# Kernel optimization log

Measured on AMD Instinct MI355X. Metric: run time of the kernel, lower is better.

Reference implementation:

```python
import jax, jax.numpy as jnp
import numpy as np

B, D, V, T = 256, 1024, 32000, 64  # num_seqs, hidden dim, vocab, history len


def setup_inputs() -> dict:
    key = jax.random.key(0)
    ks = jax.random.split(key, 8)
    hidden = jax.random.normal(ks[0], (B, D), dtype=jnp.float32)
    embedding = jax.random.normal(ks[1], (V, D), dtype=jnp.float32) * (1.0 / np.sqrt(D))
    output_tokens = jax.random.randint(ks[2], (B, T), 0, V, dtype=jnp.int64)
    presence_penalties = jax.random.uniform(ks[3], (B,), dtype=jnp.float32)
    frequency_penalties = jax.random.uniform(ks[4], (B,), dtype=jnp.float32)
    temperatures = jax.random.uniform(ks[5], (B,), dtype=jnp.float32) + 0.5  # > eps
    top_ps = jax.random.uniform(ks[6], (B,), dtype=jnp.float32) * 0.5 + 0.5  # in [0.5, 1.0)
    top_ks = jax.random.randint(ks[7], (B,), 1, V, dtype=jnp.int64)
    return {
        "hidden": hidden,
        "embedding": embedding,
        "output_tokens": output_tokens,
        "presence_penalties": presence_penalties,
        "frequency_penalties": frequency_penalties,
        "temperatures": temperatures,
        "top_ps": top_ps,
        "top_ks": top_ks,
    }


def reference(hidden, embedding, output_tokens, presence_penalties,
              frequency_penalties, temperatures, top_ps, top_ks):
    # 1) logits = pruned hidden states @ embedding^T  -> [B, V]
    logits = jnp.einsum("bd,vd->bv", hidden, embedding)
    b, v = logits.shape

    # 2) presence/frequency penalties via per-row token histogram (np.bincount equiv)
    rows = jnp.broadcast_to(jnp.arange(b)[:, None], output_tokens.shape)
    counts = jnp.zeros((b, v), logits.dtype).at[rows, output_tokens].add(1.0)
    logits = logits - frequency_penalties[:, None] * counts \
                    - presence_penalties[:, None] * (counts > 0).astype(logits.dtype)

    # 3) temperature scaling
    logits = logits / temperatures[:, None]

    # 4) probabilities
    probs = jax.nn.softmax(logits, axis=-1)

    # 5) top-p / top-k: descending sort, cumsum masks, scatter back via inverse perm
    order = jnp.argsort(-probs, axis=-1)                       # descending order
    probs_sort = jnp.take_along_axis(probs, order, axis=-1)
    probs_cum = jnp.cumsum(probs_sort, axis=-1)
    top_p_mask = (probs_cum - probs_sort) > top_ps[:, None]
    top_k_mask = jnp.arange(v)[None, :] >= top_ks[:, None]
    probs_sort = jnp.where(top_p_mask | top_k_mask, 0.0, probs_sort)
    inv = jnp.argsort(order, axis=-1)
    filtered_probs = jnp.take_along_axis(probs_sort, inv, axis=-1)  # original order
    return filtered_probs
```

## Files before the change

kernel.cpp:

```cpp
#include <hip/hip_runtime.h>
#include <math.h>

#define NB 256
#define NV 32000
#define ND 1024
#define NT 64

#define GN 64
#define BSTR 40
#define NKB 64
#define AKBF 8192
#define NGBLK (NV / GN)
#define INV2048F 4.8828125e-4f

#define NBIN 1024
#define HSTR 1032
#define HTOT (4 * HSTR)
#define FIX2 4294967296.0
#define SMASK ((1ull << 48) - 1ull)
#define SMEM_BYTES (NV * 4 + HTOT * 4)

typedef _Float16 f16x8 __attribute__((ext_vector_type(8)));
typedef _Float16 f16x4 __attribute__((ext_vector_type(4)));
typedef float f32x16 __attribute__((ext_vector_type(16)));

struct RowP2 {
  unsigned long long basePack;
  unsigned long long toppZfix;
  unsigned pfx;
  int ktop;
  float invZ;
  unsigned ustar;
  int m;
  int cEq;
};

__device__ __forceinline__ unsigned mono_enc(float f) {
  unsigned u = __float_as_uint(f);
  return (u & 0x80000000u) ? ~u : (u | 0x80000000u);
}
__device__ __forceinline__ float mono_dec(unsigned u) {
  return (u & 0x80000000u) ? __uint_as_float(u & 0x7FFFFFFFu) : __uint_as_float(~u);
}

__global__ __launch_bounds__(256) void convert_A(const float* __restrict__ hidden,
                                                 _Float16* __restrict__ A3) {
  const int g = blockIdx.x * 256 + threadIdx.x;
  const int kb = g >> 10, rem = g & 1023, r = rem >> 2, c = rem & 3;
  const float4 a4 = *(const float4*)(hidden + (size_t)r * ND + kb * 16 + c * 4);
  const float v[4] = {a4.x, a4.y, a4.z, a4.w};
  f16x4 h4, q4;
#pragma unroll
  for (int q = 0; q < 4; q++) {
    const _Float16 hh = (_Float16)v[q];
    h4[q] = hh;
    q4[q] = (_Float16)((v[q] - (float)hh) * 2048.0f);
  }
  const int s = r >> 5, l31 = r & 31;
  const int lh = c >> 1, j4 = (c & 1) * 4;
  const int lane = l31 + (lh << 5);
  _Float16* base = A3 + (size_t)kb * AKBF;
  *(f16x4*)(base + ((s * 2 + 0) * 64 + lane) * 8 + j4) = h4;
  *(f16x4*)(base + ((s * 2 + 1) * 64 + lane) * 8 + j4) = q4;
}

__global__ __launch_bounds__(256, 2) void gemm_f16s(
    const float* __restrict__ Bm, const _Float16* __restrict__ A3,
    const float* __restrict__ temp, unsigned* __restrict__ rowmax,
    float* __restrict__ C) {
  __shared__ _Float16 Bls[2][GN * BSTR];
  __shared__ float s_invT[256];
  __shared__ unsigned s_pm[256];

  const int t = threadIdx.x;
  const int l = t & 63, w = t >> 6;
  const int n0 = blockIdx.x * GN;
  s_invT[t] = 1.0f / temp[t];
  s_pm[t] = 0u;

  f32x16 accH[2][2] = {};
  f32x16 accC[2][2] = {};

  const int bn = t >> 2, bk4 = (t & 3) * 4;
  const int l31 = l & 31, lh = l >> 5;
  const int ka = lh * 8;
  const int mb = w * 64;

  const float* browp = Bm + (size_t)(n0 + bn) * ND + bk4;
  const _Float16* aB = A3 + 2048 * w + l * 8;

  f16x8 eh0, eh1, eq0, eq1;
  f16x8 oh0, oh1, oq0, oq1;

#define LOADA(P, KB)                                                  \
  do {                                                                \
    const _Float16* ap_ = aB + (size_t)(KB) * AKBF;                   \
    P##h0 = *(const f16x8*)(ap_);                                     \
    P##q0 = *(const f16x8*)(ap_ + 512);                               \
    P##h1 = *(const f16x8*)(ap_ + 1024);                              \
    P##q1 = *(const f16x8*)(ap_ + 1536);                              \
  } while (0)

#define BCONV(BV, DST)                                                \
  do {                                                                \
    f16x4 h4_, q4_;                                                   \
    const float vv_[4] = {(BV).x, (BV).y, (BV).z, (BV).w};            \
    _Pragma("unroll") for (int j_ = 0; j_ < 4; j_++) {                \
      const _Float16 h_ = (_Float16)vv_[j_];                          \
      h4_[j_] = h_;                                                   \
      q4_[j_] = (_Float16)((vv_[j_] - (float)h_) * 2048.0f);          \
    }                                                                 \
    _Float16* prow_ = (DST) + bn * BSTR;                              \
    *(f16x4*)(prow_ + bk4) = h4_;                                     \
    *(f16x4*)(prow_ + 16 + bk4) = q4_;                                \
  } while (0)

#define COMPUTE(P, CUR)                                                                     \
  do {                                                                                      \
    const _Float16* Bp_ = &Bls[CUR][0] + (size_t)l31 * BSTR + ka;                           \
    f16x8 b0h_ = *(const f16x8*)(Bp_);                                                      \
    f16x8 b1h_ = *(const f16x8*)(Bp_ + 32 * BSTR);                                          \
    accH[0][0] = __builtin_amdgcn_mfma_f32_32x32x16_f16(P##h0, b0h_, accH[0][0], 0, 0, 0);  \
    accH[0][1] = __builtin_amdgcn_mfma_f32_32x32x16_f16(P##h0, b1h_, accH[0][1], 0, 0, 0);  \
    accH[1][0] = __builtin_amdgcn_mfma_f32_32x32x16_f16(P##h1, b0h_, accH[1][0], 0, 0, 0);  \
    accH[1][1] = __builtin_amdgcn_mfma_f32_32x32x16_f16(P##h1, b1h_, accH[1][1], 0, 0, 0);  \
    f16x8 b0q_ = *(const f16x8*)(Bp_ + 16);                                                 \
    f16x8 b1q_ = *(const f16x8*)(Bp_ + 32 * BSTR + 16);                                     \
    accC[0][0] = __builtin_amdgcn_mfma_f32_32x32x16_f16(P##h0, b0q_, accC[0][0], 0, 0, 0);  \
    accC[0][1] = __builtin_amdgcn_mfma_f32_32x32x16_f16(P##h0, b1q_, accC[0][1], 0, 0, 0);  \
    accC[1][0] = __builtin_amdgcn_mfma_f32_32x32x16_f16(P##h1, b0q_, accC[1][0], 0, 0, 0);  \
    accC[1][1] = __builtin_amdgcn_mfma_f32_32x32x16_f16(P##h1, b1q_, accC[1][1], 0, 0, 0);  \
    accC[0][0] = __builtin_amdgcn_mfma_f32_32x32x16_f16(P##q0, b0h_, accC[0][0], 0, 0, 0);  \
    accC[0][1] = __builtin_amdgcn_mfma_f32_32x32x16_f16(P##q0, b1h_, accC[0][1], 0, 0, 0);  \
    accC[1][0] = __builtin_amdgcn_mfma_f32_32x32x16_f16(P##q1, b0h_, accC[1][0], 0, 0, 0);  \
    accC[1][1] = __builtin_amdgcn_mfma_f32_32x32x16_f16(P##q1, b1h_, accC[1][1], 0, 0, 0);  \
  } while (0)

  LOADA(e, 0);
  __builtin_amdgcn_sched_barrier(0);
  float4 bv0 = *(const float4*)(browp);
  __builtin_amdgcn_sched_barrier(0);
  LOADA(o, 1);
  __builtin_amdgcn_sched_barrier(0);
  float4 bvA = *(const float4*)(browp + 16);
  __builtin_amdgcn_sched_barrier(0);
  BCONV(bv0, &Bls[0][0]);
  asm volatile("s_waitcnt lgkmcnt(0)\ns_barrier" ::: "memory");

  float4 bvB;
  for (int kb = 0; kb < 62; kb += 2) {
    COMPUTE(e, 0);
    __builtin_amdgcn_sched_barrier(0);
    LOADA(e, kb + 2);
    __builtin_amdgcn_sched_barrier(0);
    bvB = *(const float4*)(browp + (size_t)(kb + 2) * 16);
    __builtin_amdgcn_sched_barrier(0);
    BCONV(bvA, &Bls[1][0]);
    asm volatile("s_waitcnt lgkmcnt(0)\ns_barrier" ::: "memory");

    COMPUTE(o, 1);
    __builtin_amdgcn_sched_barrier(0);
    LOADA(o, kb + 3);
    __builtin_amdgcn_sched_barrier(0);
    bvA = *(const float4*)(browp + (size_t)(kb + 3) * 16);
    __builtin_amdgcn_sched_barrier(0);
    BCONV(bvB, &Bls[0][0]);
    asm volatile("s_waitcnt lgkmcnt(0)\ns_barrier" ::: "memory");
  }
  COMPUTE(e, 0);
  __builtin_amdgcn_sched_barrier(0);
  BCONV(bvA, &Bls[1][0]);
  asm volatile("s_waitcnt lgkmcnt(0)\ns_barrier" ::: "memory");
  COMPUTE(o, 1);

#undef LOADA
#undef BCONV
#undef COMPUTE

#pragma unroll
  for (int mi = 0; mi < 2; mi++) {
#pragma unroll
    for (int r = 0; r < 16; r++) {
      const int row = mb + mi * 32 + (r & 3) + 8 * (r >> 2) + 4 * lh;
      const float it = s_invT[row];
      float v0 = (accH[mi][0][r] + accC[mi][0][r] * INV2048F) * it;
      float v1 = (accH[mi][1][r] + accC[mi][1][r] * INV2048F) * it;
      C[(size_t)row * NV + n0 + l31] = v0;
      C[(size_t)row * NV + n0 + 32 + l31] = v1;
      float mx = fmaxf(v0, v1);
#pragma unroll
      for (int o = 1; o < 32; o <<= 1) mx = fmaxf(mx, __shfl_xor(mx, o));
      if (l31 == 0) atomicMax(&s_pm[row], mono_enc(mx));
    }
  }
  __syncthreads();
  atomicMax(&rowmax[t], s_pm[t]);
}

__global__ __launch_bounds__(1024) void sample_row(
    float* __restrict__ buf, const unsigned* __restrict__ rowmax,
    const int* __restrict__ toks, const float* __restrict__ pres,
    const float* __restrict__ freq, const float* __restrict__ temp,
    const float* __restrict__ topp_a, const int* __restrict__ topk_a) {
  extern __shared__ char smem[];
  float* e = (float*)smem;
  unsigned* hist = (unsigned*)(smem + NV * 4);
  unsigned long long* suf = (unsigned long long*)hist;
  __shared__ unsigned long long wtot16[16];
  __shared__ int s_tok[NT];
  __shared__ int s_bs;
  __shared__ RowP2 sp;

  const int b = blockIdx.x, t = threadIdx.x;
  const int cp = (t >> 6) & 1;
  unsigned* loP = hist + cp * HSTR;
  unsigned* hcP = hist + 2 * HSTR + cp * HSTR;
  float* row = buf + (size_t)b * NV;

#define HACC(K, BIN)                                                            \
  do {                                                                          \
    unsigned long long m_ = (unsigned long long)(((K) & 0x7FFFFFu) | 0x800000u);\
    const int sh_ = (int)((K) >> 23) - 118;                                     \
    const unsigned long long f_ =                                               \
        (sh_ >= 0) ? (m_ << sh_) : ((sh_ > -24) ? (m_ >> (-sh_)) : 0ull);       \
    const unsigned flo_ = (unsigned)f_;                                         \
    const unsigned old_ = atomicAdd(&loP[BIN], flo_);                           \
    const unsigned hc_ = 0x10000u + (unsigned)(f_ >> 32) +                      \
                         ((old_ + flo_ < flo_) ? 1u : 0u);                      \
    atomicAdd(&hcP[BIN], hc_);                                                  \
  } while (0)

  if (t < NT) s_tok[t] = toks[b * NT + t];
  for (int i = t; i < HTOT; i += 1024) hist[i] = 0u;
  for (int i4 = t; i4 < NV / 4; i4 += 1024)
    *(float4*)(e + i4 * 4) = *(const float4*)(row + i4 * 4);
  __syncthreads();

  if (t < NT) {
    const int tk = s_tok[t];
    bool first = true; int cnt = 0;
    for (int j = 0; j < NT; j++)
      if (s_tok[j] == tk) { if (j < t) first = false; cnt++; }
    if (first) e[tk] -= (freq[b] * (float)cnt + pres[b]) / temp[b];
  }
  __syncthreads();

  const float M = mono_dec(rowmax[b]);
  for (int i4 = t; i4 < NV / 4; i4 += 1024) {
    float4 x4 = *(const float4*)(e + i4 * 4);
    float4 e4;
    e4.x = expf(x4.x - M); e4.y = expf(x4.y - M);
    e4.z = expf(x4.z - M); e4.w = expf(x4.w - M);
    *(float4*)(e + i4 * 4) = e4;
    unsigned k;
    k = __float_as_uint(e4.x); if (k) HACC(k, k >> 20);
    k = __float_as_uint(e4.y); if (k) HACC(k, k >> 20);
    k = __float_as_uint(e4.z); if (k) HACC(k, k >> 20);
    k = __float_as_uint(e4.w); if (k) HACC(k, k >> 20);
  }
  __syncthreads();

  const int lane = t & 63, wv = t >> 6;
  for (int level = 0; level < 3; level++) {
    const unsigned lo0 = hist[t], lo1 = hist[HSTR + t];
    const unsigned hc0 = hist[2 * HSTR + t], hc1 = hist[3 * HSTR + t];
    const unsigned c = (hc0 >> 16) + (hc1 >> 16);
    const unsigned long long sum =
        (((unsigned long long)((hc0 & 0xFFFFu) + (hc1 & 0xFFFFu))) << 32) +
        (unsigned long long)lo0 + (unsigned long long)lo1;
    unsigned long long sv = ((unsigned long long)c << 48) + sum;
#pragma unroll
    for (int off = 1; off < 64; off <<= 1) {
      const unsigned long long up = __shfl_down(sv, off, 64);
      if (lane + off < 64) sv += up;
    }
    if (lane == 0) wtot16[wv] = sv;
    if (t == 0) s_bs = NBIN - 1;
    __syncthreads();
    unsigned long long add = 0ull, tot = 0ull;
#pragma unroll
    for (int w2 = 0; w2 < 16; w2++) {
      const unsigned long long x = wtot16[w2];
      tot += x;
      add += (w2 > wv) ? x : 0ull;
    }
    const unsigned long long mySuf = sv + add;
    suf[t] = mySuf;
    const unsigned long long totalP = tot;
    __syncthreads();

    unsigned long long base, toppZ;
    int ktop_;
    if (level == 0) {
      ktop_ = topk_a[b];
      unsigned long long Zfix = totalP & SMASK;
      if (!Zfix) Zfix = 1ull;
      toppZ = (unsigned long long)((double)topp_a[b] * (double)Zfix);
      base = 0ull;
    } else {
      base = sp.basePack; toppZ = sp.toppZfix; ktop_ = sp.ktop;
    }

    {
      const unsigned long long sG = base + mySuf;
      const bool A = ((long long)(sG >> 48) < (long long)ktop_) && ((sG & SMASK) <= toppZ);
      const unsigned long long sP = base + ((t > 0) ? suf[t - 1] : totalP);
      const bool Ap = ((long long)(sP >> 48) < (long long)ktop_) && ((sP & SMASK) <= toppZ);
      if (A && !Ap) s_bs = t;
    }
    __syncthreads();
    if (t == 0) {
      const int bs = s_bs;
      const unsigned long long newBase = base + suf[bs];
      if (level == 0) {
        unsigned long long Zfix = totalP & SMASK;
        if (!Zfix) Zfix = 1ull;
        sp.invZ = (float)(FIX2 / (double)Zfix);
      }
      if (level < 2) {
        sp.basePack = newBase;
        sp.toppZfix = toppZ;
        sp.ktop = ktop_;
        sp.pfx = (level == 0) ? (unsigned)bs : ((sp.pfx << 10) | (unsigned)bs);
      } else {
        const unsigned ustar = (sp.pfx << 10) | (unsigned)bs;
        const unsigned long long raw = ((bs > 0) ? suf[bs - 1] : totalP) - suf[bs];
        const int cEq = (int)(raw >> 48);
        const long long Chi = (long long)(newBase >> 48);
        const unsigned long long Shi = newBase & SMASK;
        long long m = cEq;
        const long long lim = (long long)ktop_ - Chi;
        if (lim < m) m = lim;
        const double tf = (double)__uint_as_float(ustar) * FIX2;
        const double rem = (double)(toppZ - Shi);
        const double Rd = floor(rem / tf) + 1.0;
        if (Rd < (double)m) m = (long long)Rd;
        if (m < 1) m = 1;
        sp.ustar = ustar; sp.m = (int)m; sp.cEq = cEq;
      }
    }
    __syncthreads();

    if (level < 2) {
      for (int i = t; i < HTOT; i += 1024) hist[i] = 0u;
      __syncthreads();
      const unsigned pfx = sp.pfx;
      const int ms = (level == 0) ? 20 : 10;
      const int bsh = (level == 0) ? 10 : 0;
      for (int i4 = t; i4 < NV / 4; i4 += 1024) {
        float4 e4 = *(const float4*)(e + i4 * 4);
        unsigned k;
        k = __float_as_uint(e4.x); if (k && (k >> ms) == pfx) HACC(k, (k >> bsh) & 1023u);
        k = __float_as_uint(e4.y); if (k && (k >> ms) == pfx) HACC(k, (k >> bsh) & 1023u);
        k = __float_as_uint(e4.z); if (k && (k >> ms) == pfx) HACC(k, (k >> bsh) & 1023u);
        k = __float_as_uint(e4.w); if (k && (k >> ms) == pfx) HACC(k, (k >> bsh) & 1023u);
      }
      __syncthreads();
    }
  }
#undef HACC

  const unsigned ustar = sp.ustar;
  const float invZ = sp.invZ;
  if (sp.m >= sp.cEq) {
    for (int i4 = t; i4 < NV / 4; i4 += 1024) {
      float4 e4 = *(const float4*)(e + i4 * 4);
      float4 o4;
      unsigned k;
      k = __float_as_uint(e4.x); o4.x = (k >= ustar) ? e4.x * invZ : 0.f;
      k = __float_as_uint(e4.y); o4.y = (k >= ustar) ? e4.y * invZ : 0.f;
      k = __float_as_uint(e4.z); o4.z = (k >= ustar) ? e4.z * invZ : 0.f;
      k = __float_as_uint(e4.w); o4.w = (k >= ustar) ? e4.w * invZ : 0.f;
      *(float4*)(row + i4 * 4) = o4;
    }
  } else {
    const int m = sp.m;
    unsigned* rk = hist;
    const int base0 = t * 32;
    const int end0 = (base0 + 32 < NV) ? base0 + 32 : NV;
    int myc = 0;
    for (int v = base0; v < end0; v++)
      myc += (__float_as_uint(e[v]) == ustar);
    rk[t] = (unsigned)myc;
    __syncthreads();
    for (int off = 1; off < 1024; off <<= 1) {
      const unsigned a0 = rk[t];
      const unsigned an = (t >= off) ? rk[t - off] : 0u;
      __syncthreads();
      rk[t] = a0 + an;
      __syncthreads();
    }
    int r = (t > 0) ? (int)rk[t - 1] : 0;
    for (int v = base0; v < end0; v++) {
      const unsigned k = __float_as_uint(e[v]);
      float o = (k > ustar) ? e[v] * invZ : 0.f;
      if (k == ustar) { o = (r < m) ? e[v] * invZ : 0.f; r++; }
      row[v] = o;
    }
  }
}

extern "C" void kernel_launch(void* const* d_in, const int* in_sizes, int n_in,
                              void* d_out, int out_size, void* d_ws, size_t ws_size,
                              hipStream_t stream) {
  (void)in_sizes; (void)n_in; (void)out_size; (void)ws_size;
  const float* hidden = (const float*)d_in[0];
  const float* emb    = (const float*)d_in[1];
  const int*   toks   = (const int*)d_in[2];
  const float* pres   = (const float*)d_in[3];
  const float* freq   = (const float*)d_in[4];
  const float* temp   = (const float*)d_in[5];
  const float* topp   = (const float*)d_in[6];
  const int*   topk   = (const int*)d_in[7];
  float* out = (float*)d_out;

  const size_t offA3 = 0;
  const size_t offRM = 1048576;

  _Float16* A3 = (_Float16*)((char*)d_ws + offA3);
  unsigned* rowmax = (unsigned*)((char*)d_ws + offRM);

  hipFuncSetAttribute((const void*)sample_row,
                      hipFuncAttributeMaxDynamicSharedMemorySize, SMEM_BYTES);

  hipMemsetAsync((char*)d_ws + offRM, 0, 1024, stream);
  convert_A<<<256, 256, 0, stream>>>(hidden, A3);
  gemm_f16s<<<NGBLK, 256, 0, stream>>>(emb, A3, temp, rowmax, out);
  sample_row<<<NB, 1024, SMEM_BYTES, stream>>>(out, rowmax, toks, pres, freq,
                                               temp, topp, topk);
}
```

Before: 275.3 us.

## Drop LDS row staging in sampler and fold rowmax memset into convert kernel

The sampling kernel no longer copies each 32000-float row into shared memory. It operates directly on the global output buffer for the exp, histogram passes and final write, which frees about 128KB of LDS per block and lets more blocks be resident. The rowmax zeroing memset is folded into the convert_A kernel, removing one launch and the shared-memory attribute call. The trade is that the repeated passes over the row now hit global memory or cache instead of LDS, and the scalar tie-handling loops read global memory.

```diff
diff --git a/kernel.cpp b/kernel.cpp
--- a/kernel.cpp
+++ b/kernel.cpp
@@ -18,7 +18,6 @@
 #define HTOT (4 * HSTR)
 #define FIX2 4294967296.0
 #define SMASK ((1ull << 48) - 1ull)
-#define SMEM_BYTES (NV * 4 + HTOT * 4)
 
 typedef _Float16 f16x8 __attribute__((ext_vector_type(8)));
 typedef _Float16 f16x4 __attribute__((ext_vector_type(4)));
@@ -44,7 +43,9 @@
 }
 
 __global__ __launch_bounds__(256) void convert_A(const float* __restrict__ hidden,
-                                                 _Float16* __restrict__ A3) {
+                                                 _Float16* __restrict__ A3,
+                                                 unsigned* __restrict__ rowmax) {
+  if (blockIdx.x == 0) rowmax[threadIdx.x] = 0u;
   const int g = blockIdx.x * 256 + threadIdx.x;
   const int kb = g >> 10, rem = g & 1023, r = rem >> 2, c = rem & 3;
   const float4 a4 = *(const float4*)(hidden + (size_t)r * ND + kb * 16 + c * 4);
@@ -202,9 +203,7 @@
     const int* __restrict__ toks, const float* __restrict__ pres,
     const float* __restrict__ freq, const float* __restrict__ temp,
     const float* __restrict__ topp_a, const int* __restrict__ topk_a) {
-  extern __shared__ char smem[];
-  float* e = (float*)smem;
-  unsigned* hist = (unsigned*)(smem + NV * 4);
+  __shared__ unsigned hist[HTOT];
   unsigned long long* suf = (unsigned long long*)hist;
   __shared__ unsigned long long wtot16[16];
   __shared__ int s_tok[NT];
@@ -232,8 +231,6 @@
 
   if (t < NT) s_tok[t] = toks[b * NT + t];
   for (int i = t; i < HTOT; i += 1024) hist[i] = 0u;
-  for (int i4 = t; i4 < NV / 4; i4 += 1024)
-    *(float4*)(e + i4 * 4) = *(const float4*)(row + i4 * 4);
   __syncthreads();
 
   if (t < NT) {
@@ -241,17 +238,17 @@
     bool first = true; int cnt = 0;
     for (int j = 0; j < NT; j++)
       if (s_tok[j] == tk) { if (j < t) first = false; cnt++; }
-    if (first) e[tk] -= (freq[b] * (float)cnt + pres[b]) / temp[b];
+    if (first) row[tk] -= (freq[b] * (float)cnt + pres[b]) / temp[b];
   }
   __syncthreads();
 
   const float M = mono_dec(rowmax[b]);
   for (int i4 = t; i4 < NV / 4; i4 += 1024) {
-    float4 x4 = *(const float4*)(e + i4 * 4);
+    float4 x4 = *(const float4*)(row + i4 * 4);
     float4 e4;
     e4.x = expf(x4.x - M); e4.y = expf(x4.y - M);
     e4.z = expf(x4.z - M); e4.w = expf(x4.w - M);
-    *(float4*)(e + i4 * 4) = e4;
+    *(float4*)(row + i4 * 4) = e4;
     unsigned k;
     k = __float_as_uint(e4.x); if (k) HACC(k, k >> 20);
     k = __float_as_uint(e4.y); if (k) HACC(k, k >> 20);
@@ -348,7 +345,7 @@
       const int ms = (level == 0) ? 20 : 10;
       const int bsh = (level == 0) ? 10 : 0;
       for (int i4 = t; i4 < NV / 4; i4 += 1024) {
-        float4 e4 = *(const float4*)(e + i4 * 4);
+        float4 e4 = *(const float4*)(row + i4 * 4);
         unsigned k;
         k = __float_as_uint(e4.x); if (k && (k >> ms) == pfx) HACC(k, (k >> bsh) & 1023u);
         k = __float_as_uint(e4.y); if (k && (k >> ms) == pfx) HACC(k, (k >> bsh) & 1023u);
@@ -364,7 +361,7 @@
   const float invZ = sp.invZ;
   if (sp.m >= sp.cEq) {
     for (int i4 = t; i4 < NV / 4; i4 += 1024) {
-      float4 e4 = *(const float4*)(e + i4 * 4);
+      float4 e4 = *(const float4*)(row + i4 * 4);
       float4 o4;
       unsigned k;
       k = __float_as_uint(e4.x); o4.x = (k >= ustar) ? e4.x * invZ : 0.f;
@@ -380,7 +377,7 @@
     const int end0 = (base0 + 32 < NV) ? base0 + 32 : NV;
     int myc = 0;
     for (int v = base0; v < end0; v++)
-      myc += (__float_as_uint(e[v]) == ustar);
+      myc += (__float_as_uint(row[v]) == ustar);
     rk[t] = (unsigned)myc;
     __syncthreads();
     for (int off = 1; off < 1024; off <<= 1) {
@@ -392,9 +389,9 @@
     }
     int r = (t > 0) ? (int)rk[t - 1] : 0;
     for (int v = base0; v < end0; v++) {
-      const unsigned k = __float_as_uint(e[v]);
-      float o = (k > ustar) ? e[v] * invZ : 0.f;
-      if (k == ustar) { o = (r < m) ? e[v] * invZ : 0.f; r++; }
+      const unsigned k = __float_as_uint(row[v]);
+      float o = (k > ustar) ? row[v] * invZ : 0.f;
+      if (k == ustar) { o = (r < m) ? row[v] * invZ : 0.f; r++; }
       row[v] = o;
     }
   }
@@ -420,12 +417,8 @@
   _Float16* A3 = (_Float16*)((char*)d_ws + offA3);
   unsigned* rowmax = (unsigned*)((char*)d_ws + offRM);
 
-  hipFuncSetAttribute((const void*)sample_row,
-                      hipFuncAttributeMaxDynamicSharedMemorySize, SMEM_BYTES);
-
-  hipMemsetAsync((char*)d_ws + offRM, 0, 1024, stream);
-  convert_A<<<256, 256, 0, stream>>>(hidden, A3);
+  convert_A<<<256, 256, 0, stream>>>(hidden, A3, rowmax);
   gemm_f16s<<<NGBLK, 256, 0, stream>>>(emb, A3, temp, rowmax, out);
-  sample_row<<<NB, 1024, SMEM_BYTES, stream>>>(out, rowmax, toks, pres, freq,
-                                               temp, topp, topk);
-}
+  sample_row<<<NB, 1024, 0, stream>>>(out, rowmax, toks, pres, freq,
+                                      temp, topp, topk);
+}
```

Measured after the change: 276.6 us. Within noise of the previous version (+0.5%).
